# Kernel tuning notes

Measured on AMD Instinct MI355X. Metric: run time of the kernel, lower is better.

Reference implementation:

```python
import jax, jax.numpy as jnp
import numpy as np

DIM = 1024
HEADS = 16
DIM_HEAD = 64
INNER = HEADS * DIM_HEAD  # 1024
MAX_POS = 512
B, N = 2, 1024


def setup_inputs() -> dict:
    key = jax.random.key(0)
    ks = jax.random.split(key, 6)
    s = DIM ** -0.5
    x = jax.random.normal(ks[0], (B, N, DIM), dtype=jnp.float32)
    Wq = jax.random.normal(ks[1], (DIM, INNER), dtype=jnp.float32) * s
    Wkv = jax.random.normal(ks[2], (DIM, 2 * INNER), dtype=jnp.float32) * s
    Wo = jax.random.normal(ks[3], (INNER, DIM), dtype=jnp.float32) * (INNER ** -0.5)
    bo = jnp.zeros((DIM,), dtype=jnp.float32)
    rel_emb = jax.random.normal(ks[4], (2 * MAX_POS + 1, DIM_HEAD), dtype=jnp.float32)
    return {"x": x, "Wq": Wq, "Wkv": Wkv, "Wo": Wo, "bo": bo, "rel_emb": rel_emb}


def reference(x, Wq, Wkv, Wo, bo, rel_emb):
    b, n, _ = x.shape
    scale = DIM_HEAD ** -0.5
    q = x @ Wq                    # [b, n, inner]
    kv = x @ Wkv                  # [b, n, 2*inner]
    k, v = jnp.split(kv, 2, axis=-1)

    def split_heads(t):
        return t.reshape(b, n, HEADS, DIM_HEAD).transpose(0, 2, 1, 3)  # [b,h,n,d]

    q, k, v = map(split_heads, (q, k, v))
    dots = jnp.einsum('bhid,bhjd->bhij', q, k) * scale

    seq = jnp.arange(n)
    dist = jnp.clip(seq[:, None] - seq[None, :], -MAX_POS, MAX_POS) + MAX_POS  # [n, n]
    rel = rel_emb[dist]           # [n, n, d]
    pos_attn = jnp.einsum('bhnd,nrd->bhnr', q, rel) * scale
    dots = dots + pos_attn

    attn = jax.nn.softmax(dots, axis=-1)
    out = jnp.einsum('bhij,bhjd->bhid', attn, v)
    out = out.transpose(0, 2, 1, 3).reshape(b, n, INNER)
    return out @ Wo + bo
```

## Files before the change

### kernel.cpp

```cpp
#include <hip/hip_runtime.h>

typedef __bf16 bf16x8 __attribute__((ext_vector_type(8)));
typedef float f32x4 __attribute__((ext_vector_type(4)));

#define DEV __device__ __forceinline__

DEV unsigned short f2bf(float f) {
  union { float f; unsigned u; } x; x.f = f;
  unsigned r = x.u + 0x7FFFu + ((x.u >> 16) & 1u);
  return (unsigned short)(r >> 16);
}
DEV float bf2f(unsigned short h) {
  union { unsigned u; float f; } x; x.u = ((unsigned)h) << 16;
  return x.f;
}
DEV unsigned short bfc(float f) {
  union { __bf16 b; unsigned short u; } c; c.b = (__bf16)f; return c.u;
}

typedef __attribute__((address_space(3))) void* lds_vp;
typedef const __attribute__((address_space(1))) void* gbl_vp;
DEV void load_lds16(const unsigned short* gp, void* lp) {
  __builtin_amdgcn_global_load_lds((gbl_vp)(const void*)gp, (lds_vp)lp, 16, 0, 0);
}

__global__ __launch_bounds__(256)
void prep_k(const float* __restrict__ x, const float* __restrict__ rel,
            const float* __restrict__ bo, const float* __restrict__ Wq,
            const float* __restrict__ Wkv, const float* __restrict__ Wo,
            unsigned short* __restrict__ xb, unsigned short* __restrict__ relb,
            unsigned short* __restrict__ bob, unsigned short* __restrict__ WqkvT,
            unsigned short* __restrict__ WoT) {
  __shared__ unsigned short tile[32][33];
  const int bid = blockIdx.x, tid = threadIdx.x;
  if (bid < 2114) {
    const float* src; unsigned short* dst; long base; long n;
    if (bid < 2048)      { src = x;   dst = xb;   base = (long)bid * 1024;          n = 2097152; }
    else if (bid < 2113) { src = rel; dst = relb; base = (long)(bid - 2048) * 1024; n = 65600; }
    else                 { src = bo;  dst = bob;  base = 0;                          n = 1024; }
    long i = base + tid * 4;
    if (i < n) {
      float4 v = *(const float4*)&src[i];
      unsigned long long u = (unsigned long long)f2bf(v.x)
                           | ((unsigned long long)f2bf(v.y) << 16)
                           | ((unsigned long long)f2bf(v.z) << 32)
                           | ((unsigned long long)f2bf(v.w) << 48);
      *(unsigned long long*)&dst[i] = u;
    }
  } else {
    int id = bid - 2114;
    const float* src; unsigned short* dst; const int R = 1024; int C, txt, tyt;
    if (id < 1024)      { src = Wq;  dst = WqkvT;           C = 1024; txt = id & 31; tyt = id >> 5; }
    else if (id < 3072) { int l = id - 1024; src = Wkv; dst = WqkvT + 1048576; C = 2048; txt = l & 63; tyt = l >> 6; }
    else                { int l = id - 3072; src = Wo;  dst = WoT;             C = 1024; txt = l & 31; tyt = l >> 5; }
    int c0 = txt * 32, r0 = tyt * 32;
    int tx = tid & 31, ty = tid >> 5;
    #pragma unroll
    for (int i = 0; i < 4; ++i)
      tile[ty + i * 8][tx] = f2bf(src[(size_t)(r0 + ty + i * 8) * C + c0 + tx]);
    __syncthreads();
    #pragma unroll
    for (int i = 0; i < 4; ++i)
      dst[(size_t)(c0 + ty + i * 8) * R + r0 + tx] = tile[tx][ty + i * 8];
  }
}

DEV void stage16(const unsigned short* gbase, size_t gstride,
                 unsigned short* lbase, int r0, int lane) {
  #pragma unroll
  for (int t = 0; t < 2; ++t) {
    int r = r0 + t * 8 + (lane >> 3);
    int lc = (lane & 7) ^ (r & 7);
    load_lds16(&gbase[(size_t)r * gstride + lc * 8], &lbase[(size_t)(r0 + t * 8) * 64]);
  }
}
DEV bf16x8 read_swz(const unsigned short* buf, int row, int lc) {
  int pc = lc ^ (row & 7);
  return *(const bf16x8*)&buf[row * 64 + pc * 8];
}

__global__ __launch_bounds__(256)
void gemm_qkv(const unsigned short* __restrict__ A,
              const unsigned short* __restrict__ Bt,
              unsigned short* __restrict__ o0,
              unsigned short* __restrict__ o1,
              unsigned short* __restrict__ o2) {
  __shared__ __align__(16) unsigned short As[64 * 64];
  __shared__ __align__(16) unsigned short Bs[128 * 64];
  __shared__ unsigned short tbuf[64][68];
  const int tid  = threadIdx.x;
  const int lane = tid & 63, wave = tid >> 6;
  const int q15  = lane & 15, quad = lane >> 4;
  const int wr = wave >> 1, wc = wave & 1;
  const int m0 = blockIdx.y * 64, n0 = blockIdx.x * 128;
  const int K = 1024;

  f32x4 acc[2][4] = {};
  for (int k0 = 0; k0 < K; k0 += 64) {
    __syncthreads();
    stage16(&A[(size_t)m0 * K + k0], K, As, wave * 16, lane);
    stage16(&Bt[(size_t)n0 * K + k0], K, Bs, wave * 32, lane);
    stage16(&Bt[(size_t)n0 * K + k0], K, Bs, wave * 32 + 16, lane);
    __syncthreads();
    #pragma unroll
    for (int ks = 0; ks < 2; ++ks) {
      bf16x8 af[2], bfr[4];
      #pragma unroll
      for (int i = 0; i < 2; ++i)
        af[i] = read_swz(As, wr * 32 + i * 16 + q15, ks * 4 + quad);
      #pragma unroll
      for (int j = 0; j < 4; ++j)
        bfr[j] = read_swz(Bs, wc * 64 + j * 16 + q15, ks * 4 + quad);
      #pragma unroll
      for (int i = 0; i < 2; ++i)
        #pragma unroll
        for (int j = 0; j < 4; ++j)
          acc[i][j] = __builtin_amdgcn_mfma_f32_16x16x32_bf16(af[i], bfr[j], acc[i][j], 0, 0, 0);
    }
  }

  const int b = m0 >> 10, nn0 = m0 & 1023;
  if (n0 < 2048) {
    #pragma unroll
    for (int i = 0; i < 2; ++i)
      #pragma unroll
      for (int j = 0; j < 4; ++j)
        #pragma unroll
        for (int r = 0; r < 4; ++r) {
          int row = m0 + wr * 32 + i * 16 + quad * 4 + r;
          int col = n0 + wc * 64 + j * 16 + q15;
          float v = acc[i][j][r];
          int nn = row & 1023;
          unsigned short* dst; int c = col; float sc = 1.f;
          if (col < 1024) { dst = o0; sc = 0.125f; }
          else            { dst = o1; c = col - 1024; }
          int h = c >> 6, dd = c & 63;
          dst[((size_t)((row >> 10) * 16 + h) * 1024 + nn) * 64 + dd] = f2bf(v * sc);
        }
  } else {
    const int hp = (n0 - 2048) >> 6;
    #pragma unroll
    for (int hh = 0; hh < 2; ++hh) {
      __syncthreads();
      if (wc == hh) {
        #pragma unroll
        for (int i = 0; i < 2; ++i)
          #pragma unroll
          for (int j = 0; j < 4; ++j)
            #pragma unroll
            for (int r = 0; r < 4; ++r)
              tbuf[wr * 32 + i * 16 + quad * 4 + r][j * 16 + q15] = f2bf(acc[i][j][r]);
      }
      __syncthreads();
      const int bh = b * 16 + hp + hh;
      const int d = tid >> 2, nb = (tid & 3) * 16;
      #pragma unroll
      for (int s = 0; s < 2; ++s) {
        int n = nb + s * 8;
        union { uint4 v; unsigned short us[8]; } t;
        #pragma unroll
        for (int e = 0; e < 8; ++e) t.us[e] = tbuf[n + e][d];
        *(uint4*)&o2[((size_t)bh * 64 + d) * 1024 + nn0 + n] = t.v;
      }
    }
  }
}

__global__ __launch_bounds__(256)
void flash_attn(const unsigned short* __restrict__ q_ws,
                const unsigned short* __restrict__ k_ws,
                const unsigned short* __restrict__ vt_ws,
                const unsigned short* __restrict__ rel,
                unsigned short* __restrict__ ao) {
  __shared__ __align__(16) unsigned short Kbuf[2][64 * 64];
  __shared__ __align__(16) unsigned short Vbuf[2][64 * 64];
  __shared__ __align__(16) unsigned short P_lds[4][16 * 64];
  __shared__ __align__(16) float T_lds[4][16][84];

  const int tid  = threadIdx.x;
  const int lane = tid & 63, w = tid >> 6;
  const int q15  = lane & 15, quad = lane >> 4;
  const int bh = blockIdx.x;
  const int ib = blockIdx.y * 64 + w * 16;

  const unsigned short* qp = q_ws  + (size_t)bh * 1024 * 64;
  const unsigned short* kp = k_ws  + (size_t)bh * 1024 * 64;
  const unsigned short* tp = vt_ws + (size_t)bh * 64 * 1024;

  bf16x8 aq[2];
  #pragma unroll
  for (int ks = 0; ks < 2; ++ks)
    aq[ks] = *(const bf16x8*)&qp[(size_t)(ib + q15) * 64 + ks * 32 + quad * 8];

  f32x4 o[4] = {};
  float l_i[4] = {0.f, 0.f, 0.f, 0.f};

  stage16(kp, 64, &Kbuf[0][0], w * 16, lane);
  stage16(tp, 1024, &Vbuf[0][0], w * 16, lane);

  for (int jt = 0; jt < 16; ++jt) {
    const int j0 = jt * 64, cur = jt & 1;
    __syncthreads();
    if (jt + 1 < 16) {
      stage16(kp + (size_t)(j0 + 64) * 64, 64, &Kbuf[cur ^ 1][0], w * 16, lane);
      stage16(tp + (j0 + 64), 1024, &Vbuf[cur ^ 1][0], w * 16, lane);
    }

    f32x4 accS[4] = {};
    #pragma unroll
    for (int ks = 0; ks < 2; ++ks)
      #pragma unroll
      for (int cb = 0; cb < 4; ++cb) {
        bf16x8 bk = read_swz(&Kbuf[cur][0], cb * 16 + q15, ks * 4 + quad);
        accS[cb] = __builtin_amdgcn_mfma_f32_16x16x32_bf16(aq[ks], bk, accS[cb], 0, 0, 0);
      }
    int tb = ib - j0 + 512 - 63;
    f32x4 accT[5] = {};
    #pragma unroll
    for (int ks = 0; ks < 2; ++ks)
      #pragma unroll
      for (int ub = 0; ub < 5; ++ub) {
        int trow = tb + ub * 16 + q15;
        trow = trow < 0 ? 0 : (trow > 1024 ? 1024 : trow);
        bf16x8 br = *(const bf16x8*)&rel[(size_t)trow * 64 + ks * 32 + quad * 8];
        accT[ub] = __builtin_amdgcn_mfma_f32_16x16x32_bf16(aq[ks], br, accT[ub], 0, 0, 0);
      }
    #pragma unroll
    for (int ub = 0; ub < 5; ++ub)
      #pragma unroll
      for (int r = 0; r < 4; ++r)
        T_lds[w][quad * 4 + r][ub * 16 + q15] = accT[ub][r];

    #pragma unroll
    for (int r = 0; r < 4; ++r) {
      const int dl = quad * 4 + r;
      #pragma unroll
      for (int cb = 0; cb < 4; ++cb) {
        int dj = cb * 16 + q15;
        float s = accS[cb][r] + T_lds[w][dl][63 + dl - dj];
        float p = exp2f(fmaf(s, 1.44269504f, -64.f));
        l_i[r] += p;
        P_lds[w][dl * 64 + ((((dj >> 3) ^ (dl & 7)) << 3) | (dj & 7))] = bfc(p);
      }
    }

    #pragma unroll
    for (int ks = 0; ks < 2; ++ks) {
      bf16x8 ap = *(const bf16x8*)&P_lds[w][q15 * 64 + (((ks * 4 + quad) ^ (q15 & 7)) << 3)];
      #pragma unroll
      for (int db = 0; db < 4; ++db) {
        bf16x8 bv = read_swz(&Vbuf[cur][0], db * 16 + q15, ks * 4 + quad);
        o[db] = __builtin_amdgcn_mfma_f32_16x16x32_bf16(ap, bv, o[db], 0, 0, 0);
      }
    }
  }

  #pragma unroll
  for (int r = 0; r < 4; ++r) {
    #pragma unroll
    for (int off = 1; off < 16; off <<= 1)
      l_i[r] += __shfl_xor(l_i[r], off, 64);
    l_i[r] = 1.f / (l_i[r] + 1e-30f);
  }

  const int b = bh >> 4, h = bh & 15;
  #pragma unroll
  for (int db = 0; db < 4; ++db)
    #pragma unroll
    for (int r = 0; r < 4; ++r) {
      int row = ib + quad * 4 + r;
      ao[((size_t)(b * 1024 + row)) * 1024 + h * 64 + db * 16 + q15] =
          bfc(o[db][r] * l_i[r]);
    }
}

__global__ __launch_bounds__(256)
void gemm_out(const unsigned short* __restrict__ A,
              const unsigned short* __restrict__ Bt,
              const unsigned short* __restrict__ bias,
              float* __restrict__ fo) {
  __shared__ __align__(16) unsigned short As[64 * 64];
  __shared__ __align__(16) unsigned short Bs[64 * 64];
  const int tid  = threadIdx.x;
  const int lane = tid & 63, w = tid >> 6;
  const int q15  = lane & 15, quad = lane >> 4;
  const int m0 = blockIdx.y * 64, n0 = blockIdx.x * 64;
  const int K = 1024, N = 1024;

  f32x4 acc[4] = {};
  for (int k0 = 0; k0 < K; k0 += 64) {
    __syncthreads();
    stage16(&A[(size_t)m0 * K + k0], K, As, w * 16, lane);
    stage16(&Bt[(size_t)n0 * K + k0], K, Bs, w * 16, lane);
    __syncthreads();
    #pragma unroll
    for (int ks = 0; ks < 2; ++ks) {
      bf16x8 af = read_swz(As, w * 16 + q15, ks * 4 + quad);
      bf16x8 bfr[4];
      #pragma unroll
      for (int j = 0; j < 4; ++j)
        bfr[j] = read_swz(Bs, j * 16 + q15, ks * 4 + quad);
      #pragma unroll
      for (int j = 0; j < 4; ++j)
        acc[j] = __builtin_amdgcn_mfma_f32_16x16x32_bf16(af, bfr[j], acc[j], 0, 0, 0);
    }
  }
  #pragma unroll
  for (int j = 0; j < 4; ++j)
    #pragma unroll
    for (int r = 0; r < 4; ++r) {
      int row = m0 + w * 16 + quad * 4 + r;
      int col = n0 + j * 16 + q15;
      fo[(size_t)row * N + col] = acc[j][r] + bf2f(bias[col]);
    }
}

extern "C" void kernel_launch(void* const* d_in, const int* in_sizes, int n_in,
                              void* d_out, int out_size, void* d_ws, size_t ws_size,
                              hipStream_t stream) {
  (void)in_sizes; (void)n_in; (void)out_size; (void)ws_size;
  const float* x   = (const float*)d_in[0];
  const float* Wq  = (const float*)d_in[1];
  const float* Wkv = (const float*)d_in[2];
  const float* Wo  = (const float*)d_in[3];
  const float* bo  = (const float*)d_in[4];
  const float* rel = (const float*)d_in[5];
  float* out = (float*)d_out;

  unsigned short* ws = (unsigned short*)d_ws;
  unsigned short* WoT   = ws;
  unsigned short* relb  = WoT   + 1048576;
  unsigned short* bob   = relb  + 65664;
  unsigned short* q_ws  = bob   + 1088;
  unsigned short* k_ws  = q_ws  + 2097152;
  unsigned short* vT    = k_ws  + 2097152;
  unsigned short* WqkvT = vT    + 2097152;
  unsigned short* xb    = WqkvT + 3145728;
  unsigned short* ao    = WqkvT;

  prep_k<<<6210, 256, 0, stream>>>(x, rel, bo, Wq, Wkv, Wo,
                                   xb, relb, bob, WqkvT, WoT);
  gemm_qkv<<<dim3(24, 32), 256, 0, stream>>>(xb, WqkvT, q_ws, k_ws, vT);
  flash_attn<<<dim3(32, 16), 256, 0, stream>>>(q_ws, k_ws, vT, relb, ao);
  gemm_out<<<dim3(16, 32), 256, 0, stream>>>(ao, WoT, bob, out);
}
```

Measured before the change: 158.7 us.

## Split flash attention key range across two wave groups with LDS merge

The attention block grows to 512 threads: two groups of four waves each handle half of the key sequence, using separate K/V buffers, and their partial outputs and row sums are merged through shared memory at the end. The double-buffered prefetch is dropped in favour of a stage-then-sync pattern. The relative-position scores are stored in LDS as bf16 instead of fp32 to save space. This aims to put more waves on each CU and shorten each block's serial loop, at the cost of losing load/compute overlap, adding extra barriers, and reducing the precision of the positional term.

```diff
diff --git a/kernel.cpp b/kernel.cpp
--- a/kernel.cpp
+++ b/kernel.cpp
@@ -166,7 +166,7 @@
   }
 }
 
-__global__ __launch_bounds__(256)
+__global__ __launch_bounds__(512)
 void flash_attn(const unsigned short* __restrict__ q_ws,
                 const unsigned short* __restrict__ k_ws,
                 const unsigned short* __restrict__ vt_ws,
@@ -174,18 +174,26 @@
                 unsigned short* __restrict__ ao) {
   __shared__ __align__(16) unsigned short Kbuf[2][64 * 64];
   __shared__ __align__(16) unsigned short Vbuf[2][64 * 64];
-  __shared__ __align__(16) unsigned short P_lds[4][16 * 64];
-  __shared__ __align__(16) float T_lds[4][16][84];
+  __shared__ __align__(16) unsigned short P_lds[8][16 * 64];
+  union TXu {
+    unsigned short T[8][16][84];
+    float x[4][64][21];
+  };
+  __shared__ __align__(16) TXu tx;
 
   const int tid  = threadIdx.x;
   const int lane = tid & 63, w = tid >> 6;
   const int q15  = lane & 15, quad = lane >> 4;
+  const int wr4  = w & 3, jh = w >> 2;
   const int bh = blockIdx.x;
-  const int ib = blockIdx.y * 64 + w * 16;
+  const int ib = blockIdx.y * 64 + wr4 * 16;
 
   const unsigned short* qp = q_ws  + (size_t)bh * 1024 * 64;
   const unsigned short* kp = k_ws  + (size_t)bh * 1024 * 64;
   const unsigned short* tp = vt_ws + (size_t)bh * 64 * 1024;
+
+  unsigned short* Kb = &Kbuf[jh][0];
+  unsigned short* Vb = &Vbuf[jh][0];
 
   bf16x8 aq[2];
   #pragma unroll
@@ -195,25 +203,12 @@
   f32x4 o[4] = {};
   float l_i[4] = {0.f, 0.f, 0.f, 0.f};
 
-  stage16(kp, 64, &Kbuf[0][0], w * 16, lane);
-  stage16(tp, 1024, &Vbuf[0][0], w * 16, lane);
-
-  for (int jt = 0; jt < 16; ++jt) {
-    const int j0 = jt * 64, cur = jt & 1;
-    __syncthreads();
-    if (jt + 1 < 16) {
-      stage16(kp + (size_t)(j0 + 64) * 64, 64, &Kbuf[cur ^ 1][0], w * 16, lane);
-      stage16(tp + (j0 + 64), 1024, &Vbuf[cur ^ 1][0], w * 16, lane);
-    }
-
-    f32x4 accS[4] = {};
-    #pragma unroll
-    for (int ks = 0; ks < 2; ++ks)
-      #pragma unroll
-      for (int cb = 0; cb < 4; ++cb) {
-        bf16x8 bk = read_swz(&Kbuf[cur][0], cb * 16 + q15, ks * 4 + quad);
-        accS[cb] = __builtin_amdgcn_mfma_f32_16x16x32_bf16(aq[ks], bk, accS[cb], 0, 0, 0);
-      }
+  for (int jt = 0; jt < 8; ++jt) {
+    const int j0 = jh * 512 + jt * 64;
+    __syncthreads();
+    stage16(kp + (size_t)j0 * 64, 64, Kb, wr4 * 16, lane);
+    stage16(tp + j0, 1024, Vb, wr4 * 16, lane);
+
     int tb = ib - j0 + 512 - 63;
     f32x4 accT[5] = {};
     #pragma unroll
@@ -229,7 +224,18 @@
     for (int ub = 0; ub < 5; ++ub)
       #pragma unroll
       for (int r = 0; r < 4; ++r)
-        T_lds[w][quad * 4 + r][ub * 16 + q15] = accT[ub][r];
+        tx.T[w][quad * 4 + r][ub * 16 + q15] = bfc(accT[ub][r]);
+
+    __syncthreads();
+
+    f32x4 accS[4] = {};
+    #pragma unroll
+    for (int ks = 0; ks < 2; ++ks)
+      #pragma unroll
+      for (int cb = 0; cb < 4; ++cb) {
+        bf16x8 bk = read_swz(Kb, cb * 16 + q15, ks * 4 + quad);
+        accS[cb] = __builtin_amdgcn_mfma_f32_16x16x32_bf16(aq[ks], bk, accS[cb], 0, 0, 0);
+      }
 
     #pragma unroll
     for (int r = 0; r < 4; ++r) {
@@ -237,7 +243,7 @@
       #pragma unroll
       for (int cb = 0; cb < 4; ++cb) {
         int dj = cb * 16 + q15;
-        float s = accS[cb][r] + T_lds[w][dl][63 + dl - dj];
+        float s = accS[cb][r] + bf2f(tx.T[w][dl][63 + dl - dj]);
         float p = exp2f(fmaf(s, 1.44269504f, -64.f));
         l_i[r] += p;
         P_lds[w][dl * 64 + ((((dj >> 3) ^ (dl & 7)) << 3) | (dj & 7))] = bfc(p);
@@ -249,29 +255,47 @@
       bf16x8 ap = *(const bf16x8*)&P_lds[w][q15 * 64 + (((ks * 4 + quad) ^ (q15 & 7)) << 3)];
       #pragma unroll
       for (int db = 0; db < 4; ++db) {
-        bf16x8 bv = read_swz(&Vbuf[cur][0], db * 16 + q15, ks * 4 + quad);
+        bf16x8 bv = read_swz(Vb, db * 16 + q15, ks * 4 + quad);
         o[db] = __builtin_amdgcn_mfma_f32_16x16x32_bf16(ap, bv, o[db], 0, 0, 0);
       }
     }
   }
 
   #pragma unroll
-  for (int r = 0; r < 4; ++r) {
+  for (int r = 0; r < 4; ++r)
     #pragma unroll
     for (int off = 1; off < 16; off <<= 1)
       l_i[r] += __shfl_xor(l_i[r], off, 64);
-    l_i[r] = 1.f / (l_i[r] + 1e-30f);
-  }
-
-  const int b = bh >> 4, h = bh & 15;
-  #pragma unroll
-  for (int db = 0; db < 4; ++db)
-    #pragma unroll
-    for (int r = 0; r < 4; ++r) {
-      int row = ib + quad * 4 + r;
-      ao[((size_t)(b * 1024 + row)) * 1024 + h * 64 + db * 16 + q15] =
-          bfc(o[db][r] * l_i[r]);
-    }
+
+  __syncthreads();
+
+  if (w >= 4) {
+    float* xr = tx.x[w - 4][lane];
+    #pragma unroll
+    for (int db = 0; db < 4; ++db)
+      #pragma unroll
+      for (int r = 0; r < 4; ++r)
+        xr[db * 4 + r] = o[db][r];
+    #pragma unroll
+    for (int r = 0; r < 4; ++r) xr[16 + r] = l_i[r];
+  }
+  __syncthreads();
+  if (w < 4) {
+    const float* xr = tx.x[w][lane];
+    float inv[4];
+    #pragma unroll
+    for (int r = 0; r < 4; ++r)
+      inv[r] = 1.f / (l_i[r] + xr[16 + r] + 1e-30f);
+    const int b = bh >> 4, h = bh & 15;
+    #pragma unroll
+    for (int db = 0; db < 4; ++db)
+      #pragma unroll
+      for (int r = 0; r < 4; ++r) {
+        int row = ib + quad * 4 + r;
+        ao[((size_t)(b * 1024 + row)) * 1024 + h * 64 + db * 16 + q15] =
+            bfc((o[db][r] + xr[db * 4 + r]) * inv[r]);
+      }
+  }
 }
 
 __global__ __launch_bounds__(256)
@@ -341,6 +365,6 @@
   prep_k<<<6210, 256, 0, stream>>>(x, rel, bo, Wq, Wkv, Wo,
                                    xb, relb, bob, WqkvT, WoT);
   gemm_qkv<<<dim3(24, 32), 256, 0, stream>>>(xb, WqkvT, q_ws, k_ws, vT);
-  flash_attn<<<dim3(32, 16), 256, 0, stream>>>(q_ws, k_ws, vT, relb, ao);
+  flash_attn<<<dim3(32, 16), 512, 0, stream>>>(q_ws, k_ws, vT, relb, ao);
   gemm_out<<<dim3(16, 32), 256, 0, stream>>>(ao, WoT, bob, out);
 }
```

After: 157.5 us. Within noise of the previous version (-0.8%).
